# Kernel optimization log

Hardware: AMD Instinct MI355X
Metric: run time of the kernel (lower is better)

Reference implementation:

```python
import jax, jax.numpy as jnp
import numpy as np

B, N, C, M, OUT = 4, 256, 32, 4, 64


def _uniform(k, shape, fan_in):
    s = 1.0 / np.sqrt(fan_in)
    return jax.random.uniform(k, shape, jnp.float32, -s, s)


def setup_inputs() -> dict:
    key = jax.random.key(0)
    ks = jax.random.split(key, 11)
    return {
        "x": jax.random.normal(ks[0], (B, N, N, C), jnp.float32),
        # Neighborhood / SnConv2to1 linears (in=C, out=M neighborhood channels)
        "w1_nb": _uniform(ks[1], (3 * C, M), 3 * C),
        "b1_nb": _uniform(ks[2], (M,), 3 * C),
        "w0_nb": _uniform(ks[3], (2 * C, M), 2 * C),
        "b0_nb": _uniform(ks[4], (M,), 2 * C),
        # SnConv2 linears (in channels = M*C after neighborhood product)
        "w2d": _uniform(ks[5], (2 * M * C, OUT), 2 * M * C),
        "b2d": _uniform(ks[6], (OUT,), 2 * M * C),
        "w1d": _uniform(ks[7], (3 * M * C, OUT), 3 * M * C),
        "b1d": _uniform(ks[8], (OUT,), 3 * M * C),
        "w0d": _uniform(ks[9], (2 * M * C, OUT), 2 * M * C),
        "b0d": _uniform(ks[10], (OUT,), 2 * M * C),
    }


def _contractions(x):
    # x: [B, n, n, c]; mask=None, reduction='mean' path of _get_contractions
    n = x.shape[1]
    rowsum = x.sum(axis=1) / n                      # [B, n, c]
    colsum = x.sum(axis=2) / n                      # [B, n, c]
    diag = jnp.diagonal(x, axis1=1, axis2=2)        # [B, c, n]
    rowcolsum = x.sum(axis=(1, 2)) / (n * n)        # [B, c]
    diag_sum = diag.sum(axis=-1) / n                # [B, c]  (/= sqrt(n^2))
    diag = jnp.moveaxis(diag, -1, 1)                # move_from_end -> [B, n, c]
    return rowsum, colsum, diag, rowcolsum, diag_sum


def reference(x, w1_nb, b1_nb, w0_nb, b0_nb, w2d, b2d, w1d, b1d, w0d, b0d):
    # ---- Neighborhood: SnConv2to1 -> sigmoid ----
    rs, cs, dg, rcs, ds = _contractions(x)
    obj1 = jnp.concatenate([rs, cs, dg], axis=-1)             # [B, n, 3C]
    obj0 = jnp.concatenate([rcs, ds], axis=-1)                # [B, 2C]
    node = obj1 @ w1_nb + b1_nb + (obj0 @ w0_nb + b0_nb)[:, None, :]
    neighbs = jax.nn.sigmoid(node)                            # [B, n, M]
    # ---- _neighbor_elementwise_product ----
    expanded = neighbs[:, None, :, :] * neighbs[:, :, None, :]  # [B, n, n, M]
    # channel_product: outer product over channel dims, collapsed to M*C
    xl = (expanded[..., :, None] * x[..., None, :]).reshape(B, N, N, M * C)
    # ---- SnConv2 on the localized tensor ----
    rs2, cs2, dg2, rcs2, ds2 = _contractions(xl)
    obj2d = jnp.concatenate([xl, jnp.swapaxes(xl, 1, 2)], axis=-1)  # [B,n,n,2MC]
    obj1d = jnp.concatenate([rs2, cs2, dg2], axis=-1)               # [B,n,3MC]
    obj0d = jnp.concatenate([rcs2, ds2], axis=-1)                   # [B,2MC]
    out = (obj2d @ w2d + b2d
           + (obj1d @ w1d + b1d)[:, None, :, :]
           + (obj0d @ w0d + b0d)[:, None, None, :])                 # [B,n,n,OUT]
    return out
```

## Files before the change

### kernel.cpp

```cpp
#include <hip/hip_runtime.h>
#include <math.h>

#define Bv 4
#define Nv 256
#define Cv 32
#define Mv 4
#define OUTv 64
#define MCv (Mv*Cv)

typedef _Float16 h8 __attribute__((ext_vector_type(8)));
typedef _Float16 h4 __attribute__((ext_vector_type(4)));
typedef float f4 __attribute__((ext_vector_type(4)));

__device__ __align__(16) float g_rs  [Bv * Nv * Cv];
__device__ __align__(16) float g_cs  [Bv * Nv * Cv];
__device__ __align__(16) float g_dgx [Bv * Nv * Cv];
__device__ __align__(16) float g_nb  [Bv * Nv * Mv];
__device__ __align__(16) float g_S1  [Bv * Nv * MCv];
__device__ __align__(16) float g_S2  [Bv * Nv * MCv];
__device__ __align__(16) float g_rcs2[Bv * MCv];
__device__ __align__(16) float g_ds2 [Bv * MCv];
__device__ __align__(16) float g_addv[Bv * Nv * OUTv];
__device__ __align__(16) _Float16 g_wfrag[8 * 4 * 64 * 8];

__global__ __launch_bounds__(256) void k_contract1(const float* __restrict__ x,
                                                   const float* __restrict__ w2d) {
    int bx = blockIdx.x, b = blockIdx.y;
    int t = threadIdx.x;
    if (bx >= 2 * Nv) {
        if (b != 0) return;
        int r = bx - 2 * Nv;
        if (r == 8) {
            if (t < 128) ((float4*)g_rcs2)[t] = {0.f,0.f,0.f,0.f};
            else         ((float4*)g_ds2)[t - 128] = {0.f,0.f,0.f,0.f};
            return;
        }
        int fi = r * 256 + t;
        int s = fi >> 8, q = (fi >> 6) & 3, lane = fi & 63;
        int k0 = s * 32 + ((lane >> 4) << 3);
        int o = q * 16 + (lane & 15);
        #pragma unroll
        for (int jj = 0; jj < 8; jj++)
            g_wfrag[fi * 8 + jj] = (_Float16)w2d[(size_t)(k0 + jj) * OUTv + o];
        return;
    }
    int c4 = t & 7, sub = t >> 3;
    const float4* xb4 = (const float4*)(x + (size_t)b * Nv * Nv * Cv);
    __shared__ float red[32][36];
    float4 acc = {0.f,0.f,0.f,0.f};
    if (bx < Nv) {
        int n = bx;
        for (int i = sub; i < Nv; i += 32) {
            float4 v = xb4[((size_t)i * Nv + n) * 8 + c4];
            acc.x += v.x; acc.y += v.y; acc.z += v.z; acc.w += v.w;
        }
        red[sub][c4*4+0] = acc.x; red[sub][c4*4+1] = acc.y;
        red[sub][c4*4+2] = acc.z; red[sub][c4*4+3] = acc.w;
        __syncthreads();
        if (t < 32) {
            float s = 0.f;
            #pragma unroll
            for (int k = 0; k < 32; k++) s += red[k][t];
            g_rs[(b * Nv + n) * Cv + t] = s * (1.0f / Nv);
        }
        if (t < 8) ((float4*)g_dgx)[(b * Nv + n) * 8 + t] = xb4[((size_t)n * Nv + n) * 8 + t];
    } else {
        int n = bx - Nv;
        for (int j = sub; j < Nv; j += 32) {
            float4 v = xb4[((size_t)n * Nv + j) * 8 + c4];
            acc.x += v.x; acc.y += v.y; acc.z += v.z; acc.w += v.w;
        }
        red[sub][c4*4+0] = acc.x; red[sub][c4*4+1] = acc.y;
        red[sub][c4*4+2] = acc.z; red[sub][c4*4+3] = acc.w;
        __syncthreads();
        if (t < 32) {
            float s = 0.f;
            #pragma unroll
            for (int k = 0; k < 32; k++) s += red[k][t];
            g_cs[(b * Nv + n) * Cv + t] = s * (1.0f / Nv);
        }
    }
}

__global__ void k_neighb(const float* __restrict__ w1, const float* __restrict__ b1,
                         const float* __restrict__ w0, const float* __restrict__ b0) {
    int b = blockIdx.x, t = threadIdx.x;
    int c = t & 31, sub = t >> 5;
    float ar = 0.f, ad = 0.f;
    for (int n = sub; n < Nv; n += 8) {
        ar += g_rs[(b * Nv + n) * Cv + c];
        ad += g_dgx[(b * Nv + n) * Cv + c];
    }
    __shared__ float red[8][64];
    __shared__ float obj0[64];
    __shared__ float t0nb[4];
    red[sub][c] = ar;
    red[sub][32 + c] = ad;
    __syncthreads();
    if (t < 64) {
        float s = 0.f;
        #pragma unroll
        for (int k = 0; k < 8; k++) s += red[k][t];
        obj0[t] = s * (1.0f / Nv);
    }
    __syncthreads();
    if (t < 4) {
        float v = b0[t];
        for (int k = 0; k < 2 * Cv; k++) v += obj0[k] * w0[k * Mv + t];
        t0nb[t] = v;
    }
    __syncthreads();
    int n = t;
    float node[4];
    #pragma unroll
    for (int m = 0; m < 4; m++) node[m] = t0nb[m] + b1[m];
    for (int cc = 0; cc < Cv; cc++) {
        float r = g_rs[(b * Nv + n) * Cv + cc];
        float s = g_cs[(b * Nv + n) * Cv + cc];
        float d = g_dgx[(b * Nv + n) * Cv + cc];
        #pragma unroll
        for (int m = 0; m < 4; m++)
            node[m] += r * w1[cc * Mv + m] + s * w1[(Cv + cc) * Mv + m] + d * w1[(2 * Cv + cc) * Mv + m];
    }
    #pragma unroll
    for (int m = 0; m < 4; m++)
        g_nb[(b * Nv + n) * Mv + m] = 1.0f / (1.0f + expf(-node[m]));
}

__global__ __launch_bounds__(256) void k_wsum(const float* __restrict__ x) {
    int bx = blockIdx.x, b = blockIdx.y;
    int t = threadIdx.x, c4 = t & 7, sub = t >> 3;
    __shared__ __align__(16) float4 nbl[Nv];
    if (t < Nv) nbl[t] = ((const float4*)(g_nb + (size_t)b * Nv * Mv))[t];
    __syncthreads();
    const float4* xb4 = (const float4*)(x + (size_t)b * Nv * Nv * Cv);
    float4 a[4];
    #pragma unroll
    for (int m = 0; m < 4; m++) a[m] = {0.f,0.f,0.f,0.f};
    __shared__ float red[32][132];
    if (bx < Nv) {
        int n = bx;
        for (int i = sub; i < Nv; i += 32) {
            float4 v = xb4[((size_t)i * Nv + n) * 8 + c4];
            float4 nv = nbl[i];
            a[0].x += nv.x*v.x; a[0].y += nv.x*v.y; a[0].z += nv.x*v.z; a[0].w += nv.x*v.w;
            a[1].x += nv.y*v.x; a[1].y += nv.y*v.y; a[1].z += nv.y*v.z; a[1].w += nv.y*v.w;
            a[2].x += nv.z*v.x; a[2].y += nv.z*v.y; a[2].z += nv.z*v.z; a[2].w += nv.z*v.w;
            a[3].x += nv.w*v.x; a[3].y += nv.w*v.y; a[3].z += nv.w*v.z; a[3].w += nv.w*v.w;
        }
        #pragma unroll
        for (int m = 0; m < 4; m++) {
            red[sub][m*32 + c4*4+0] = a[m].x; red[sub][m*32 + c4*4+1] = a[m].y;
            red[sub][m*32 + c4*4+2] = a[m].z; red[sub][m*32 + c4*4+3] = a[m].w;
        }
        __syncthreads();
        if (t < 128) {
            float s = 0.f;
            #pragma unroll
            for (int k = 0; k < 32; k++) s += red[k][t];
            g_S1[(size_t)(b * Nv + n) * MCv + t] = s;
            int m = t >> 5, c = t & 31;
            float nv = ((const float*)&nbl[n])[m];
            atomicAdd(&g_rcs2[b * MCv + t], nv * s);
            atomicAdd(&g_ds2 [b * MCv + t], nv * nv * g_dgx[(b * Nv + n) * Cv + c]);
        }
    } else {
        int n = bx - Nv;
        for (int j = sub; j < Nv; j += 32) {
            float4 v = xb4[((size_t)n * Nv + j) * 8 + c4];
            float4 nv = nbl[j];
            a[0].x += nv.x*v.x; a[0].y += nv.x*v.y; a[0].z += nv.x*v.z; a[0].w += nv.x*v.w;
            a[1].x += nv.y*v.x; a[1].y += nv.y*v.y; a[1].z += nv.y*v.z; a[1].w += nv.y*v.w;
            a[2].x += nv.z*v.x; a[2].y += nv.z*v.y; a[2].z += nv.z*v.z; a[2].w += nv.z*v.w;
            a[3].x += nv.w*v.x; a[3].y += nv.w*v.y; a[3].z += nv.w*v.z; a[3].w += nv.w*v.w;
        }
        #pragma unroll
        for (int m = 0; m < 4; m++) {
            red[sub][m*32 + c4*4+0] = a[m].x; red[sub][m*32 + c4*4+1] = a[m].y;
            red[sub][m*32 + c4*4+2] = a[m].z; red[sub][m*32 + c4*4+3] = a[m].w;
        }
        __syncthreads();
        if (t < 128) {
            float s = 0.f;
            #pragma unroll
            for (int k = 0; k < 32; k++) s += red[k][t];
            g_S2[(size_t)(b * Nv + n) * MCv + t] = s;
        }
    }
}

__global__ __launch_bounds__(256) void k_add(const float* __restrict__ w1d,
                                             const float* __restrict__ b1d,
                                             const float* __restrict__ b2d,
                                             const float* __restrict__ w0d,
                                             const float* __restrict__ b0d) {
    int b = blockIdx.y, n = blockIdx.x;
    int t = threadIdx.x, o = t & 63, ks = t >> 6;
    __shared__ float red[4][64];
    const float invN = 1.0f / Nv;
    const float invN2 = invN * invN;
    float nv = g_nb[(b * Nv + n) * Mv + ks];
    float f = nv * invN, d2 = nv * nv;
    const float* S1r = g_S1 + (size_t)(b * Nv + n) * MCv + ks * 32;
    const float* S2r = g_S2 + (size_t)(b * Nv + n) * MCv + ks * 32;
    const float* dgr = g_dgx + (size_t)(b * Nv + n) * Cv;
    const float* rcr = g_rcs2 + b * MCv + ks * 32;
    const float* dsr = g_ds2  + b * MCv + ks * 32;
    float acc = 0.f;
    #pragma unroll 8
    for (int c = 0; c < 32; c++) {
        int mc = ks * 32 + c;
        acc += f * S1r[c] * w1d[(size_t)mc * OUTv + o]
             + f * S2r[c] * w1d[(size_t)(MCv + mc) * OUTv + o]
             + d2 * dgr[c] * w1d[(size_t)(2 * MCv + mc) * OUTv + o]
             + invN2 * rcr[c] * w0d[(size_t)mc * OUTv + o]
             + invN  * dsr[c] * w0d[(size_t)(MCv + mc) * OUTv + o];
    }
    red[ks][o] = acc;
    __syncthreads();
    if (t < 64) {
        float v = red[0][t] + red[1][t] + red[2][t] + red[3][t]
                + b1d[t] + b2d[t] + b0d[t];
        g_addv[(size_t)(b * Nv + n) * OUTv + t] = v;
    }
}

#define XPAD 40
__global__ __launch_bounds__(256) void k_main(const float* __restrict__ x,
                                              float* __restrict__ out) {
    int jt = blockIdx.x, i = blockIdx.y, b = blockIdx.z;
    int j0 = jt * 128;
    int t = threadIdx.x;
    int lane = t & 63, w = t >> 6;
    int rowA = lane & 15, quad = lane >> 4;

    __shared__ __align__(16) _Float16 Xt[128 * XPAD];
    __shared__ __align__(16) _Float16 Xb[128 * XPAD];

    {
        const float4* x4 = (const float4*)x;
        #pragma unroll
        for (int r = 0; r < 4; r++) {
            int idx = r * 256 + t;
            int j = idx >> 3, c4 = idx & 7;
            float4 v = x4[((size_t)(b * Nv + i) * Nv + j0 + j) * 8 + c4];
            h4 hv; hv[0] = (_Float16)v.x; hv[1] = (_Float16)v.y;
            hv[2] = (_Float16)v.z; hv[3] = (_Float16)v.w;
            *(h4*)&Xt[j * XPAD + c4 * 4] = hv;
            float4 u = x4[((size_t)(b * Nv + j0 + j) * Nv + i) * 8 + c4];
            h4 hu; hu[0] = (_Float16)u.x; hu[1] = (_Float16)u.y;
            hu[2] = (_Float16)u.z; hu[3] = (_Float16)u.w;
            *(h4*)&Xb[j * XPAD + c4 * 4] = hu;
        }
    }
    int jl1 = w * 32 + rowA, jl2 = jl1 + 16;
    _Float16 e1h[4], e2h[4];
    {
        const float* ni = g_nb + (size_t)(b * Nv + i) * Mv;
        const float* n1 = g_nb + (size_t)(b * Nv + j0 + jl1) * Mv;
        const float* n2 = g_nb + (size_t)(b * Nv + j0 + jl2) * Mv;
        #pragma unroll
        for (int m = 0; m < 4; m++) {
            e1h[m] = (_Float16)(ni[m] * n1[m]);
            e2h[m] = (_Float16)(ni[m] * n2[m]);
        }
    }
    __syncthreads();

    f4 acc[2][4];
    #pragma unroll
    for (int js = 0; js < 2; js++)
        #pragma unroll
        for (int q = 0; q < 4; q++) acc[js][q] = {0.f, 0.f, 0.f, 0.f};

    const h8* Wf = (const h8*)g_wfrag;
    #pragma unroll
    for (int part = 0; part < 2; part++) {
        const _Float16* X = part ? Xb : Xt;
        h8 xv1 = *(const h8*)&X[jl1 * XPAD + quad * 8];
        h8 xv2 = *(const h8*)&X[jl2 * XPAD + quad * 8];
        #pragma unroll
        for (int m = 0; m < 4; m++) {
            h8 a1 = xv1 * e1h[m];
            h8 a2 = xv2 * e2h[m];
            int s = part * 4 + m;
            #pragma unroll
            for (int q = 0; q < 4; q++) {
                h8 bf = Wf[(s * 4 + q) * 64 + lane];
                acc[0][q] = __builtin_amdgcn_mfma_f32_16x16x32_f16(a1, bf, acc[0][q], 0, 0, 0);
                acc[1][q] = __builtin_amdgcn_mfma_f32_16x16x32_f16(a2, bf, acc[1][q], 0, 0, 0);
            }
        }
    }
    #pragma unroll
    for (int js = 0; js < 2; js++) {
        int jbase = j0 + w * 32 + js * 16 + quad * 4;
        #pragma unroll
        for (int q = 0; q < 4; q++) {
            int o = q * 16 + rowA;
            #pragma unroll
            for (int r = 0; r < 4; r++) {
                int j = jbase + r;
                float v = acc[js][q][r] + g_addv[(size_t)(b * Nv + j) * OUTv + o];
                out[(((size_t)(b * Nv + i)) * Nv + j) * OUTv + o] = v;
            }
        }
    }
}

extern "C" void kernel_launch(void* const* d_in, const int* in_sizes, int n_in,
                              void* d_out, int out_size, void* d_ws, size_t ws_size,
                              hipStream_t stream) {
    const float* x     = (const float*)d_in[0];
    const float* w1_nb = (const float*)d_in[1];
    const float* b1_nb = (const float*)d_in[2];
    const float* w0_nb = (const float*)d_in[3];
    const float* b0_nb = (const float*)d_in[4];
    const float* w2d   = (const float*)d_in[5];
    const float* b2d   = (const float*)d_in[6];
    const float* w1d   = (const float*)d_in[7];
    const float* b1d   = (const float*)d_in[8];
    const float* w0d   = (const float*)d_in[9];
    const float* b0d   = (const float*)d_in[10];
    float* out = (float*)d_out;
    (void)d_ws; (void)ws_size;

    hipLaunchKernelGGL(k_contract1, dim3(2 * Nv + 9, Bv), dim3(256), 0, stream, x, w2d);
    hipLaunchKernelGGL(k_neighb, dim3(Bv), dim3(256), 0, stream,
                       w1_nb, b1_nb, w0_nb, b0_nb);
    hipLaunchKernelGGL(k_wsum, dim3(2 * Nv, Bv), dim3(256), 0, stream, x);
    hipLaunchKernelGGL(k_add, dim3(Nv, Bv), dim3(256), 0, stream,
                       w1d, b1d, b2d, w0d, b0d);
    hipLaunchKernelGGL(k_main, dim3(2, Nv, Bv), dim3(256), 0, stream, x, out);
}
```

Baseline: 190.9 us.

## Replicate rcs2 atomics, move ds2 sum to neighb, pair rows in k_add, stage weights in LDS

Several changes at once. The rcs2 atomic accumulator is split into 8 replicas indexed by n to cut atomic contention, and the replicas are summed in k_add. The ds2 reduction moves out of k_wsum atomics into a deterministic shared-memory reduction in k_neighb. k_add now handles two rows per block so weight loads are reused, and k_main copies the fp16 weight fragments into LDS instead of reading them from global memory. The costs are extra LDS use in k_main, which may lower occupancy, and more serial work in the single-block-per-batch k_neighb.

```diff
diff --git a/kernel.cpp b/kernel.cpp
--- a/kernel.cpp
+++ b/kernel.cpp
@@ -18,7 +18,7 @@
 __device__ __align__(16) float g_nb  [Bv * Nv * Mv];
 __device__ __align__(16) float g_S1  [Bv * Nv * MCv];
 __device__ __align__(16) float g_S2  [Bv * Nv * MCv];
-__device__ __align__(16) float g_rcs2[Bv * MCv];
+__device__ __align__(16) float g_rcs2R[8 * Bv * MCv];
 __device__ __align__(16) float g_ds2 [Bv * MCv];
 __device__ __align__(16) float g_addv[Bv * Nv * OUTv];
 __device__ __align__(16) _Float16 g_wfrag[8 * 4 * 64 * 8];
@@ -31,8 +31,9 @@
         if (b != 0) return;
         int r = bx - 2 * Nv;
         if (r == 8) {
-            if (t < 128) ((float4*)g_rcs2)[t] = {0.f,0.f,0.f,0.f};
-            else         ((float4*)g_ds2)[t - 128] = {0.f,0.f,0.f,0.f};
+            float4 z = {0.f,0.f,0.f,0.f};
+            #pragma unroll
+            for (int k = 0; k < 4; k++) ((float4*)g_rcs2R)[k * 256 + t] = z;
             return;
         }
         int fi = r * 256 + t;
@@ -94,6 +95,8 @@
     __shared__ float red[8][64];
     __shared__ float obj0[64];
     __shared__ float t0nb[4];
+    __shared__ float nbs[Nv][4];
+    __shared__ float dsred[2][128];
     red[sub][c] = ar;
     red[sub][32 + c] = ad;
     __syncthreads();
@@ -123,8 +126,25 @@
             node[m] += r * w1[cc * Mv + m] + s * w1[(Cv + cc) * Mv + m] + d * w1[(2 * Cv + cc) * Mv + m];
     }
     #pragma unroll
-    for (int m = 0; m < 4; m++)
-        g_nb[(b * Nv + n) * Mv + m] = 1.0f / (1.0f + expf(-node[m]));
+    for (int m = 0; m < 4; m++) {
+        float sg = 1.0f / (1.0f + expf(-node[m]));
+        nbs[t][m] = sg;
+        g_nb[(b * Nv + n) * Mv + m] = sg;
+    }
+    __syncthreads();
+    {
+        int mc = t & 127, h = t >> 7;
+        int m = mc >> 5, cc = mc & 31;
+        float s = 0.f;
+        for (int k = 0; k < 128; k++) {
+            int nn = h * 128 + k;
+            float nv = nbs[nn][m];
+            s += nv * nv * g_dgx[(b * Nv + nn) * Cv + cc];
+        }
+        dsred[h][mc] = s;
+    }
+    __syncthreads();
+    if (t < 128) g_ds2[b * MCv + t] = dsred[0][t] + dsred[1][t];
 }
 
 __global__ __launch_bounds__(256) void k_wsum(const float* __restrict__ x) {
@@ -159,10 +179,9 @@
             #pragma unroll
             for (int k = 0; k < 32; k++) s += red[k][t];
             g_S1[(size_t)(b * Nv + n) * MCv + t] = s;
-            int m = t >> 5, c = t & 31;
+            int m = t >> 5;
             float nv = ((const float*)&nbl[n])[m];
-            atomicAdd(&g_rcs2[b * MCv + t], nv * s);
-            atomicAdd(&g_ds2 [b * MCv + t], nv * nv * g_dgx[(b * Nv + n) * Cv + c]);
+            atomicAdd(&g_rcs2R[(((n & 7) * Bv) + b) * MCv + t], nv * s);
         }
     } else {
         int n = bx - Nv;
@@ -194,34 +213,55 @@
                                              const float* __restrict__ b2d,
                                              const float* __restrict__ w0d,
                                              const float* __restrict__ b0d) {
-    int b = blockIdx.y, n = blockIdx.x;
+    int b = blockIdx.y, n0 = blockIdx.x * 2;
     int t = threadIdx.x, o = t & 63, ks = t >> 6;
-    __shared__ float red[4][64];
+    __shared__ float rcl[MCv], dsl[MCv];
+    __shared__ float red0[4][64];
+    __shared__ float red2[4][2][64];
+    if (t < 128) {
+        float s = 0.f;
+        #pragma unroll
+        for (int r = 0; r < 8; r++) s += g_rcs2R[(r * Bv + b) * MCv + t];
+        rcl[t] = s;
+    } else {
+        dsl[t - 128] = g_ds2[b * MCv + (t - 128)];
+    }
+    __syncthreads();
     const float invN = 1.0f / Nv;
     const float invN2 = invN * invN;
-    float nv = g_nb[(b * Nv + n) * Mv + ks];
-    float f = nv * invN, d2 = nv * nv;
-    const float* S1r = g_S1 + (size_t)(b * Nv + n) * MCv + ks * 32;
-    const float* S2r = g_S2 + (size_t)(b * Nv + n) * MCv + ks * 32;
-    const float* dgr = g_dgx + (size_t)(b * Nv + n) * Cv;
-    const float* rcr = g_rcs2 + b * MCv + ks * 32;
-    const float* dsr = g_ds2  + b * MCv + ks * 32;
-    float acc = 0.f;
+    float nv0 = g_nb[(b * Nv + n0) * Mv + ks];
+    float nv1 = g_nb[(b * Nv + n0 + 1) * Mv + ks];
+    float f0 = nv0 * invN, d20 = nv0 * nv0;
+    float f1 = nv1 * invN, d21 = nv1 * nv1;
+    const float* S1a = g_S1 + (size_t)(b * Nv + n0) * MCv + ks * 32;
+    const float* S1b = S1a + MCv;
+    const float* S2a = g_S2 + (size_t)(b * Nv + n0) * MCv + ks * 32;
+    const float* S2b = S2a + MCv;
+    const float* dga = g_dgx + (size_t)(b * Nv + n0) * Cv;
+    const float* dgb = dga + Cv;
+    float acc0v = 0.f, accA = 0.f, accB = 0.f;
     #pragma unroll 8
-    for (int c = 0; c < 32; c++) {
-        int mc = ks * 32 + c;
-        acc += f * S1r[c] * w1d[(size_t)mc * OUTv + o]
-             + f * S2r[c] * w1d[(size_t)(MCv + mc) * OUTv + o]
-             + d2 * dgr[c] * w1d[(size_t)(2 * MCv + mc) * OUTv + o]
-             + invN2 * rcr[c] * w0d[(size_t)mc * OUTv + o]
-             + invN  * dsr[c] * w0d[(size_t)(MCv + mc) * OUTv + o];
-    }
-    red[ks][o] = acc;
-    __syncthreads();
-    if (t < 64) {
-        float v = red[0][t] + red[1][t] + red[2][t] + red[3][t]
-                + b1d[t] + b2d[t] + b0d[t];
-        g_addv[(size_t)(b * Nv + n) * OUTv + t] = v;
+    for (int cc = 0; cc < 32; cc++) {
+        int mc = ks * 32 + cc;
+        float w1a = w1d[(size_t)mc * OUTv + o];
+        float w1b = w1d[(size_t)(MCv + mc) * OUTv + o];
+        float w1c = w1d[(size_t)(2 * MCv + mc) * OUTv + o];
+        float w0a = w0d[(size_t)mc * OUTv + o];
+        float w0b = w0d[(size_t)(MCv + mc) * OUTv + o];
+        acc0v += invN2 * rcl[mc] * w0a + invN * dsl[mc] * w0b;
+        accA  += f0 * S1a[cc] * w1a + f0 * S2a[cc] * w1b + d20 * dga[cc] * w1c;
+        accB  += f1 * S1b[cc] * w1a + f1 * S2b[cc] * w1b + d21 * dgb[cc] * w1c;
+    }
+    red0[ks][o] = acc0v;
+    red2[ks][0][o] = accA;
+    red2[ks][1][o] = accB;
+    __syncthreads();
+    if (t < 128) {
+        int nn = t >> 6, oo = t & 63;
+        float t0v = red0[0][oo] + red0[1][oo] + red0[2][oo] + red0[3][oo]
+                  + b1d[oo] + b2d[oo] + b0d[oo];
+        float v = red2[0][nn][oo] + red2[1][nn][oo] + red2[2][nn][oo] + red2[3][nn][oo] + t0v;
+        g_addv[(size_t)(b * Nv + n0 + nn) * OUTv + oo] = v;
     }
 }
 
@@ -234,9 +274,16 @@
     int lane = t & 63, w = t >> 6;
     int rowA = lane & 15, quad = lane >> 4;
 
+    __shared__ __align__(16) _Float16 Wl[8 * 4 * 64 * 8];
     __shared__ __align__(16) _Float16 Xt[128 * XPAD];
     __shared__ __align__(16) _Float16 Xb[128 * XPAD];
 
+    {
+        const float4* src = (const float4*)g_wfrag;
+        float4* dst = (float4*)Wl;
+        #pragma unroll
+        for (int r = 0; r < 8; r++) dst[r * 256 + t] = src[r * 256 + t];
+    }
     {
         const float4* x4 = (const float4*)x;
         #pragma unroll
@@ -273,7 +320,7 @@
         #pragma unroll
         for (int q = 0; q < 4; q++) acc[js][q] = {0.f, 0.f, 0.f, 0.f};
 
-    const h8* Wf = (const h8*)g_wfrag;
+    const h8* Wf = (const h8*)Wl;
     #pragma unroll
     for (int part = 0; part < 2; part++) {
         const _Float16* X = part ? Xb : Xt;
@@ -329,7 +376,7 @@
     hipLaunchKernelGGL(k_neighb, dim3(Bv), dim3(256), 0, stream,
                        w1_nb, b1_nb, w0_nb, b0_nb);
     hipLaunchKernelGGL(k_wsum, dim3(2 * Nv, Bv), dim3(256), 0, stream, x);
-    hipLaunchKernelGGL(k_add, dim3(Nv, Bv), dim3(256), 0, stream,
+    hipLaunchKernelGGL(k_add, dim3(Nv / 2, Bv), dim3(256), 0, stream,
                        w1d, b1d, b2d, w0d, b0d);
     hipLaunchKernelGGL(k_main, dim3(2, Nv, Bv), dim3(256), 0, stream, x, out);
 }
```

Result: faster. 173.6 us (-9.1%).
